# Kernel tuning notes

Hardware: AMD Instinct MI355X
Metric: run time of the kernel (lower is better)

The kernel has to match this reference:

```python
import jax, jax.numpy as jnp
import numpy as np

D_MODEL = 2048
NUM_HEADS = 16
HEAD_DIM = 128
ROPE_BASE = 10000.0
NEG_INF = -1e9


def setup_inputs() -> dict:
    key = jax.random.key(0)
    ks = jax.random.split(key, 5)
    B, S = 2, 2048
    hidden_states = jax.random.normal(ks[0], (B, S, D_MODEL), dtype=jnp.float32)
    # additive causal mask: 0 on/below diagonal, large-negative above
    causal = jnp.triu(jnp.full((S, S), NEG_INF, dtype=jnp.float32), k=1)
    attention_mask = jnp.broadcast_to(causal, (B, 1, S, S))
    position_ids = jnp.broadcast_to(jnp.arange(S, dtype=jnp.int32), (B, S))
    scale = 1.0 / np.sqrt(D_MODEL)
    Wq = jax.random.normal(ks[1], (D_MODEL, NUM_HEADS * HEAD_DIM), dtype=jnp.float32) * scale
    Wk = jax.random.normal(ks[2], (D_MODEL, NUM_HEADS * HEAD_DIM), dtype=jnp.float32) * scale
    Wv = jax.random.normal(ks[3], (D_MODEL, NUM_HEADS * HEAD_DIM), dtype=jnp.float32) * scale
    Wo = jax.random.normal(ks[4], (NUM_HEADS * HEAD_DIM, D_MODEL), dtype=jnp.float32) * scale
    return {"hidden_states": hidden_states, "attention_mask": attention_mask,
            "position_ids": position_ids, "Wq": Wq, "Wk": Wk, "Wv": Wv, "Wo": Wo}


def _rope_cos_sin(position_ids):
    # inv_freq: [head_dim/2]
    inv_freq = 1.0 / (ROPE_BASE ** (jnp.arange(0, HEAD_DIM, 2, dtype=jnp.float32) / HEAD_DIM))
    freqs = position_ids.astype(jnp.float32)[..., None] * inv_freq  # [B,S,hd/2]
    emb = jnp.concatenate([freqs, freqs], axis=-1)  # [B,S,hd]
    return jnp.cos(emb), jnp.sin(emb)


def _rotate_half(x):
    x1, x2 = jnp.split(x, 2, axis=-1)
    return jnp.concatenate([-x2, x1], axis=-1)


def reference(hidden_states, attention_mask, position_ids, Wq, Wk, Wv, Wo):
    B, S, _ = hidden_states.shape
    H, Dh = NUM_HEADS, HEAD_DIM
    q = (hidden_states @ Wq).reshape(B, S, H, Dh).transpose(0, 2, 1, 3)  # [B,H,S,Dh]
    k = (hidden_states @ Wk).reshape(B, S, H, Dh).transpose(0, 2, 1, 3)
    v = (hidden_states @ Wv).reshape(B, S, H, Dh).transpose(0, 2, 1, 3)
    cos, sin = _rope_cos_sin(position_ids)  # [B,S,Dh]
    cos = cos[:, None, :, :]  # [B,1,S,Dh]
    sin = sin[:, None, :, :]
    q = q * cos + _rotate_half(q) * sin
    k = k * cos + _rotate_half(k) * sin
    scaling = 1.0 / np.sqrt(Dh)
    scores = jnp.einsum('bhqd,bhkd->bhqk', q, k) * scaling  # [B,H,S,S]
    scores = scores + attention_mask[:, :, :, :S]
    attn = jax.nn.softmax(scores.astype(jnp.float32), axis=-1).astype(q.dtype)
    # dropout p=0.0 / eval mode -> identity
    out = jnp.einsum('bhqk,bhkd->bhqd', attn, v)  # [B,H,S,Dh]
    out = out.transpose(0, 2, 1, 3).reshape(B, S, H * Dh)
    return out @ Wo
```

## Files before the change

kernel.cpp:

```cpp
#include <hip/hip_runtime.h>

typedef __attribute__((ext_vector_type(4))) float f32x4;
typedef __attribute__((ext_vector_type(8))) _Float16 f16x8;
typedef __attribute__((ext_vector_type(4))) _Float16 f16x4;

#define SEQ 2048
#define DM 2048
#define NQKV 6144

__device__ __forceinline__ void gload16(const _Float16* g, _Float16* l) {
  __builtin_amdgcn_global_load_lds(
      (const __attribute__((address_space(1))) void*)g,
      (__attribute__((address_space(3))) void*)l, 16, 0, 0);
}

__global__ __launch_bounds__(256) void cvt_x_kernel(const float* __restrict__ X,
                                                    _Float16* __restrict__ Xb, int n4) {
  int i = blockIdx.x * 256 + threadIdx.x;
  if (i < n4) {
    const float4 v = ((const float4*)X)[i];
    f16x4 o;
    o.x = (_Float16)v.x; o.y = (_Float16)v.y; o.z = (_Float16)v.z; o.w = (_Float16)v.w;
    ((f16x4*)Xb)[i] = o;
  }
}

__global__ __launch_bounds__(256) void wtrans_all_kernel(const float* __restrict__ Wq,
                                                         const float* __restrict__ Wk,
                                                         const float* __restrict__ Wv,
                                                         const float* __restrict__ Wo,
                                                         _Float16* __restrict__ Wqkvt,
                                                         _Float16* __restrict__ Wot) {
  __shared__ float tile[64][65];
  const int z = blockIdx.z;
  const float* W = (z == 0) ? Wq : (z == 1) ? Wk : (z == 2) ? Wv : Wo;
  _Float16* Wt = (z < 3) ? (Wqkvt + (size_t)z * 2048 * 2048) : Wot;
  const int n0 = blockIdx.x * 64, k0 = blockIdx.y * 64;
  const int tx = threadIdx.x & 15, ty = threadIdx.x >> 4;
#pragma unroll
  for (int i = 0; i < 4; ++i) {
    const int r = ty + i * 16;
    const float4 v = *(const float4*)&W[(size_t)(k0 + r) * 2048 + n0 + tx * 4];
    tile[r][tx * 4] = v.x; tile[r][tx * 4 + 1] = v.y;
    tile[r][tx * 4 + 2] = v.z; tile[r][tx * 4 + 3] = v.w;
  }
  __syncthreads();
  const int r = threadIdx.x >> 2, u = threadIdx.x & 3;
  _Float16 o[16];
#pragma unroll
  for (int i = 0; i < 16; ++i) o[i] = (_Float16)tile[u * 16 + i][r];
  _Float16* dst = &Wt[(size_t)(n0 + r) * 2048 + k0 + u * 16];
  *(f16x8*)&dst[0] = *(f16x8*)&o[0];
  *(f16x8*)&dst[8] = *(f16x8*)&o[8];
}

__global__ __launch_bounds__(256) void rope_table_kernel(float* __restrict__ ct,
                                                         float* __restrict__ st) {
  int i = blockIdx.x * 256 + threadIdx.x;
  int pos = i >> 6, f = i & 63;
  float inv = powf(10000.0f, -(float)f / 64.0f);
  float ang = (float)pos * inv;
  ct[i] = cosf(ang);
  st[i] = sinf(ang);
}

template <int MODE>
__global__ __launch_bounds__(512, 2) void gemm8n_kernel(
    const _Float16* __restrict__ A, const _Float16* __restrict__ Bt,
    float* __restrict__ Cout, int M, int N, int K,
    const int* __restrict__ pos_ids, const float* __restrict__ ct,
    const float* __restrict__ st, _Float16* __restrict__ Qo,
    _Float16* __restrict__ Ko, _Float16* __restrict__ Vo) {
  __shared__ __align__(16) char smem[147456];
  _Float16* As = (_Float16*)smem;
  _Float16* Bs = (_Float16*)(smem + 98304);
  const int nwg = gridDim.x * gridDim.y;
  const int orig = blockIdx.y * gridDim.x + blockIdx.x;
  const int id = (orig & 7) * (nwg >> 3) + (orig >> 3);
  const int bx = id % gridDim.x, by = id / gridDim.x;
  const int bm = by * 256, bn = bx * 128;
  const int t = threadIdx.x, lane = t & 63, w = t >> 6;
  const int wm = w >> 2, wn = w & 3;
  const int rl = lane & 15, lr4 = lane >> 4;
  const int NKT = K >> 6;

  const int srow = t >> 3;
  const int scol = ((t & 7) ^ (srow & 7)) << 3;
  const _Float16* pA = A + (size_t)(bm + srow) * K + scol;
  const _Float16* pB = Bt + (size_t)(bn + srow) * K + scol;
  _Float16* lA = As + t * 8;
  _Float16* lB = Bs + t * 8;
  const size_t rowK64 = (size_t)64 * K;

#define STA(H, KT, SLOT)                                                   \
  { const size_t _g = (size_t)((H) * 128) * K + (size_t)(KT) * 64;         \
    gload16(pA + _g, lA + (SLOT) * 16384 + (H) * 8192);                    \
    gload16(pA + _g + rowK64, lA + (SLOT) * 16384 + (H) * 8192 + 4096); }
#define STB(KT, SLOT)                                                      \
  { const size_t _g = (size_t)(KT) * 64;                                   \
    gload16(pB + _g, lB + (SLOT) * 8192);                                  \
    gload16(pB + _g + rowK64, lB + (SLOT) * 8192 + 4096); }

  const int sw0 = (lr4 ^ (rl & 7)) << 3;
  const int sw1 = ((4 + lr4) ^ (rl & 7)) << 3;
  const int aoff = (wm * 64 + rl) * 64;
  const int boff = (wn * 32 + rl) * 64;

  f16x8 a_[4][2], b_[2][2];
  f32x4 acc[2][4][2];
#pragma unroll
  for (int qm = 0; qm < 2; ++qm)
#pragma unroll
    for (int mf = 0; mf < 4; ++mf)
#pragma unroll
      for (int nf = 0; nf < 2; ++nf) acc[qm][mf][nf] = (f32x4)0.0f;

#define LOAD_A(H, SLOT)                                                 \
  { const _Float16* _p = As + (SLOT) * 16384 + (H) * 8192 + aoff;       \
    _Pragma("unroll") for (int mf = 0; mf < 4; ++mf) {                  \
      a_[mf][0] = *(const f16x8*)&_p[mf * 1024 + sw0];                  \
      a_[mf][1] = *(const f16x8*)&_p[mf * 1024 + sw1]; } }
#define LOAD_B(SLOT)                                                    \
  { const _Float16* _p = Bs + (SLOT) * 8192 + boff;                     \
    _Pragma("unroll") for (int nf = 0; nf < 2; ++nf) {                  \
      b_[nf][0] = *(const f16x8*)&_p[nf * 1024 + sw0];                  \
      b_[nf][1] = *(const f16x8*)&_p[nf * 1024 + sw1]; } }
#define MFMA_Q(QM)                                                      \
  __builtin_amdgcn_s_setprio(1);                                        \
  _Pragma("unroll") for (int mf = 0; mf < 4; ++mf)                      \
    _Pragma("unroll") for (int nf = 0; nf < 2; ++nf) {                  \
      acc[QM][mf][nf] = __builtin_amdgcn_mfma_f32_16x16x32_f16(         \
          a_[mf][0], b_[nf][0], acc[QM][mf][nf], 0, 0, 0);              \
      acc[QM][mf][nf] = __builtin_amdgcn_mfma_f32_16x16x32_f16(         \
          a_[mf][1], b_[nf][1], acc[QM][mf][nf], 0, 0, 0); }            \
  __builtin_amdgcn_s_setprio(0);
#define BAR()                                                           \
  do { __builtin_amdgcn_sched_barrier(0); __builtin_amdgcn_s_barrier(); \
       __builtin_amdgcn_sched_barrier(0); } while (0)
#define LGKM0()                                                         \
  do { asm volatile("s_waitcnt lgkmcnt(0)" ::: "memory");               \
       __builtin_amdgcn_sched_barrier(0); } while (0)
#define VM6() asm volatile("s_waitcnt vmcnt(6)" ::: "memory")
#define VM0() asm volatile("s_waitcnt vmcnt(0)" ::: "memory")

  STA(0, 0, 0); STB(0, 0); STA(1, 0, 0);
  STA(0, 1, 1); STB(1, 1); STA(1, 1, 1);
  VM6();
  BAR();

  for (int jb = 0; jb + 4 < NKT; jb += 3) {
    LOAD_A(0, 0); LOAD_B(0); STA(0, jb + 2, 2); STB(jb + 2, 2);
    BAR(); LGKM0(); MFMA_Q(0); BAR();
    LOAD_A(1, 0); STA(1, jb + 2, 2);
    VM6(); BAR(); LGKM0(); MFMA_Q(1); BAR();
    LOAD_A(0, 1); LOAD_B(1); STA(0, jb + 3, 0); STB(jb + 3, 0);
    BAR(); LGKM0(); MFMA_Q(0); BAR();
    LOAD_A(1, 1); STA(1, jb + 3, 0);
    VM6(); BAR(); LGKM0(); MFMA_Q(1); BAR();
    LOAD_A(0, 2); LOAD_B(2); STA(0, jb + 4, 1); STB(jb + 4, 1);
    BAR(); LGKM0(); MFMA_Q(0); BAR();
    LOAD_A(1, 2); STA(1, jb + 4, 1);
    VM6(); BAR(); LGKM0(); MFMA_Q(1); BAR();
  }
  {
    LOAD_A(0, 0); LOAD_B(0);
    BAR(); LGKM0(); MFMA_Q(0); BAR();
    LOAD_A(1, 0);
    VM0();
    BAR(); LGKM0(); MFMA_Q(1); BAR();
    LOAD_A(0, 1); LOAD_B(1);
    BAR(); LGKM0(); MFMA_Q(0); BAR();
    LOAD_A(1, 1);
    BAR(); LGKM0(); MFMA_Q(1);
  }

  if (MODE == 0) {
#pragma unroll
    for (int qm = 0; qm < 2; ++qm)
#pragma unroll
      for (int mf = 0; mf < 4; ++mf)
#pragma unroll
        for (int nf = 0; nf < 2; ++nf) {
          const int col = bn + wn * 32 + nf * 16 + rl;
#pragma unroll
          for (int ri = 0; ri < 4; ++ri) {
            const int row = bm + qm * 128 + wm * 64 + mf * 16 + lr4 * 4 + ri;
            Cout[(size_t)row * N + col] = acc[qm][mf][nf][ri];
          }
        }
  } else {
    const int ttype = bx >> 4;
    const int hh = bx & 15;
    if (ttype == 2) {
#pragma unroll
      for (int qm = 0; qm < 2; ++qm)
#pragma unroll
        for (int mf = 0; mf < 4; ++mf)
#pragma unroll
          for (int nf = 0; nf < 2; ++nf) {
            const int d = wn * 32 + nf * 16 + rl;
            const int s0 = bm + qm * 128 + wm * 64 + mf * 16 + lr4 * 4;
            const int bb = s0 >> 11, ss = s0 & 2047;
            f16x4 v4;
#pragma unroll
            for (int ri = 0; ri < 4; ++ri) v4[ri] = (_Float16)acc[qm][mf][nf][ri];
            *(f16x4*)&Vo[((size_t)(bb * 16 + hh) * 128 + d) * SEQ + ss] = v4;
          }
    } else {
      float* cl = (float*)smem;
      LGKM0();
      BAR();
#pragma unroll
      for (int qm = 0; qm < 2; ++qm)
#pragma unroll
        for (int mf = 0; mf < 4; ++mf)
#pragma unroll
          for (int nf = 0; nf < 2; ++nf) {
            const int col = wn * 32 + nf * 16 + rl;
            const int r0 = qm * 128 + wm * 64 + mf * 16 + lr4 * 4;
#pragma unroll
            for (int ri = 0; ri < 4; ++ri) cl[(r0 + ri) * 130 + col] = acc[qm][mf][nf][ri];
          }
      BAR();
      const int row = t >> 1, pb = (t & 1) * 32;
      const int rg = bm + row;
      const int bb = rg >> 11, ss = rg & 2047;
      const int pos = pos_ids[rg];
      const float* cp = ct + pos * 64 + pb;
      const float* sp = st + pos * 64 + pb;
      _Float16* dst = (ttype ? Ko : Qo) + ((size_t)(bb * 16 + hh) * SEQ + ss) * 128;
      const float qs = ttype ? 1.0f : 0.08838834764831845f;
      const float* crow = cl + row * 130;
      _Float16 o1[32], o2[32];
#pragma unroll
      for (int i = 0; i < 32; ++i) {
        const float x1 = crow[pb + i], x2 = crow[pb + 64 + i];
        const float c = cp[i], s = sp[i];
        o1[i] = (_Float16)((x1 * c - x2 * s) * qs);
        o2[i] = (_Float16)((x2 * c + x1 * s) * qs);
      }
#pragma unroll
      for (int i = 0; i < 4; ++i) {
        *(f16x8*)&dst[pb + i * 8] = *(f16x8*)&o1[i * 8];
        *(f16x8*)&dst[pb + 64 + i * 8] = *(f16x8*)&o2[i * 8];
      }
    }
  }
#undef STA
#undef STB
#undef LOAD_A
#undef LOAD_B
#undef MFMA_Q
#undef BAR
#undef LGKM0
#undef VM6
#undef VM0
}

__global__ __launch_bounds__(512) void attn_kernel(const _Float16* __restrict__ Q,
                                                   const _Float16* __restrict__ K,
                                                   const _Float16* __restrict__ Vt,
                                                   _Float16* __restrict__ O) {
  __shared__ __align__(16) _Float16 Ks[2][128 * 128];
  __shared__ __align__(16) _Float16 Vs[2][128 * 128];
  __shared__ __align__(16) _Float16 Ps[8][16 * 128];
  const int bh = blockIdx.x;
  const int pair = blockIdx.y;
  const int b = bh >> 4, h = bh & 15;
  const int t = threadIdx.x, lane = t & 63, w = t >> 6;
  const int lr = lane >> 4, lc = lane & 15;
  const _Float16* Qb = Q + (size_t)bh * SEQ * 128;
  const _Float16* Kb = K + (size_t)bh * SEQ * 128;
  const _Float16* Vb = Vt + (size_t)bh * 128 * SEQ;

  f16x8 onef;
#pragma unroll
  for (int i = 0; i < 8; ++i) onef[i] = (_Float16)1.0f;

#define ABAR()                                                          \
  do { __builtin_amdgcn_sched_barrier(0); __builtin_amdgcn_s_barrier(); \
       __builtin_amdgcn_sched_barrier(0); } while (0)

  auto stage = [&](int buf, int kb) {
    const int k0 = kb * 128;
#pragma unroll
    for (int i = 0; i < 4; ++i) {
      const int c = i * 512 + t;
      const int row = c >> 4, u = c & 15;
      gload16(&Kb[(size_t)(k0 + row) * 128 + ((u ^ (row & 7)) << 3)], &Ks[buf][c * 8]);
    }
#pragma unroll
    for (int i = 0; i < 4; ++i) {
      const int c = i * 512 + t;
      const int dim = c >> 4, u = c & 15;
      gload16(&Vb[(size_t)dim * SEQ + k0 + ((u ^ (dim & 7)) << 3)], &Vs[buf][c * 8]);
    }
  };

  for (int half = 0; half < 2; ++half) {
    const int j = half ? (15 - pair) : pair;
    const int q0 = j * 128;
    const int nkb = j + 1;
    const int rowmin = q0 + w * 16;

    f16x8 qf[4];
    {
      const int qrow = q0 + w * 16 + lc;
#pragma unroll
      for (int kk = 0; kk < 4; ++kk)
        qf[kk] = *(const f16x8*)&Qb[(size_t)qrow * 128 + kk * 32 + lr * 8];
    }
    f32x4 acco[8];
#pragma unroll
    for (int i = 0; i < 8; ++i) acco[i] = (f32x4)0.0f;
    float l_r[4] = {0.f, 0.f, 0.f, 0.f};

    stage(0, 0);
    for (int kb = 0; kb < nkb; ++kb) {
      const int cur = kb & 1;
      const bool more = kb + 1 < nkb;
      if (more) {
        stage(cur ^ 1, kb + 1);
        asm volatile("s_waitcnt vmcnt(8)" ::: "memory");
      } else {
        asm volatile("s_waitcnt vmcnt(0)" ::: "memory");
      }
      ABAR();
      const int k0 = kb * 128;
      if (k0 <= rowmin + 15) {
        f32x4 sacc[8];
#pragma unroll
        for (int jj = 0; jj < 8; ++jj) sacc[jj] = (f32x4)0.0f;
#pragma unroll
        for (int jj = 0; jj < 8; ++jj) {
          const int krow = jj * 16 + lc;
#pragma unroll
          for (int kk = 0; kk < 4; ++kk) {
            const int idx = (krow * 128 + kk * 32 + lr * 8) ^ ((krow & 7) << 3);
            f16x8 kf = *(const f16x8*)&Ks[cur][idx];
            sacc[jj] = __builtin_amdgcn_mfma_f32_16x16x32_f16(qf[kk], kf, sacc[jj], 0, 0, 0);
          }
        }
        const bool diag = (k0 + 127 > rowmin);
#pragma unroll
        for (int r = 0; r < 4; ++r) {
          const int rowi = rowmin + lr * 4 + r;
          const int rbase = (lr * 4 + r) * 128;
          const int rsw = ((lr * 4 + r) & 7) << 3;
#pragma unroll
          for (int jj = 0; jj < 8; ++jj) {
            float sv = sacc[jj][r];
            if (diag && (k0 + jj * 16 + lc > rowi)) sv = -1e30f;
            const float pv = __expf(sv);
            Ps[w][rbase + ((jj * 16 + lc) ^ rsw)] = (_Float16)pv;
          }
        }
        const int csw = (lc & 7) << 3;
        f16x8 pf[4];
#pragma unroll
        for (int c = 0; c < 4; ++c)
          pf[c] = *(const f16x8*)&Ps[w][lc * 128 + ((c * 32 + lr * 8) ^ csw)];
        f32x4 psum = (f32x4)0.0f;
#pragma unroll
        for (int c = 0; c < 4; ++c)
          psum = __builtin_amdgcn_mfma_f32_16x16x32_f16(pf[c], onef, psum, 0, 0, 0);
#pragma unroll
        for (int tt = 0; tt < 8; ++tt) {
          const int dim = tt * 16 + lc;
          const int dsw = (dim & 7) << 3;
#pragma unroll
          for (int c = 0; c < 4; ++c) {
            const int vidx = (dim * 128 + c * 32 + lr * 8) ^ dsw;
            acco[tt] = __builtin_amdgcn_mfma_f32_16x16x32_f16(
                pf[c], *(const f16x8*)&Vs[cur][vidx], acco[tt], 0, 0, 0);
          }
        }
#pragma unroll
        for (int r = 0; r < 4; ++r) l_r[r] += psum[r];
      }
      ABAR();
    }
#pragma unroll
    for (int tt = 0; tt < 8; ++tt) {
      const int col = h * 128 + tt * 16 + lc;
#pragma unroll
      for (int r = 0; r < 4; ++r) {
        const int row = q0 + w * 16 + lr * 4 + r;
        O[(size_t)(b * SEQ + row) * DM + col] = (_Float16)(acco[tt][r] / l_r[r]);
      }
    }
  }
#undef ABAR
}

extern "C" void kernel_launch(void* const* d_in, const int* in_sizes, int n_in,
                              void* d_out, int out_size, void* d_ws, size_t ws_size,
                              hipStream_t stream) {
  const float* hidden = (const float*)d_in[0];
  const int* pos_ids = (const int*)d_in[2];
  const float* Wq = (const float*)d_in[3];
  const float* Wk = (const float*)d_in[4];
  const float* Wv = (const float*)d_in[5];
  const float* Wo = (const float*)d_in[6];

  char* ws = (char*)d_ws;
  _Float16* Xb    = (_Float16*)(ws + 0);
  _Float16* Wqkvt = (_Float16*)(ws + 16777216);
  _Float16* Wot   = (_Float16*)(ws + 41943040);
  _Float16* Qbuf  = (_Float16*)(ws + 50331648);
  _Float16* Kbuf  = (_Float16*)(ws + 67108864);
  _Float16* Vtbuf = (_Float16*)(ws + 83886080);
  _Float16* Obuf  = (_Float16*)(ws + 100663296);
  float* ct       = (float*)(ws + 117440512);
  float* st       = (float*)(ws + 117964800);

  cvt_x_kernel<<<8192, 256, 0, stream>>>(hidden, Xb, 2097152);
  wtrans_all_kernel<<<dim3(32, 32, 4), 256, 0, stream>>>(Wq, Wk, Wv, Wo, Wqkvt, Wot);
  rope_table_kernel<<<512, 256, 0, stream>>>(ct, st);

  gemm8n_kernel<1><<<dim3(48, 16), 512, 0, stream>>>(
      Xb, Wqkvt, nullptr, 4096, 6144, 2048, pos_ids, ct, st, Qbuf, Kbuf, Vtbuf);

  attn_kernel<<<dim3(32, 8), 512, 0, stream>>>(Qbuf, Kbuf, Vtbuf, Obuf);

  gemm8n_kernel<0><<<dim3(16, 16), 512, 0, stream>>>(
      Obuf, Wot, (float*)d_out, 4096, 2048, 2048, nullptr, nullptr, nullptr,
      nullptr, nullptr, nullptr);
}
```

Baseline: 257.5 us.

## Use 256x256 tiles with double-buffered schedule for fused QKV projection GEMM

Adds a dedicated QKV GEMM kernel that computes 256x256 output tiles per workgroup, covering two heads, instead of 256x128. It uses a two-stage LDS buffer with interleaved A/B loads and keeps two sets of B fragments in registers. The aim is to cut global and LDS traffic per FLOP and to halve the grid to 384 workgroups. The RoPE/V-transpose epilogue is reworked to handle two heads per tile in two passes. The cost is more accumulator registers (128 floats per thread), which risks spills or lower occupancy, and less pipeline depth.

```diff
diff --git a/kernel.cpp b/kernel.cpp
--- a/kernel.cpp
+++ b/kernel.cpp
@@ -64,16 +64,217 @@
   st[i] = sinf(ang);
 }
 
-template <int MODE>
+#define BARX()                                                          \
+  do { __builtin_amdgcn_sched_barrier(0); __builtin_amdgcn_s_barrier(); \
+       __builtin_amdgcn_sched_barrier(0); } while (0)
+#define LGKM0X()                                                        \
+  do { asm volatile("s_waitcnt lgkmcnt(0)" ::: "memory");               \
+       __builtin_amdgcn_sched_barrier(0); } while (0)
+
+__global__ __launch_bounds__(512, 2) void gemm8q_kernel(
+    const _Float16* __restrict__ A, const _Float16* __restrict__ Bt,
+    int M, int N, int K, const int* __restrict__ pos_ids,
+    const float* __restrict__ ct, const float* __restrict__ st,
+    _Float16* __restrict__ Qo, _Float16* __restrict__ Ko,
+    _Float16* __restrict__ Vo) {
+  __shared__ __align__(16) char smem[135168];
+  _Float16* As = (_Float16*)smem;
+  _Float16* Bs = (_Float16*)(smem + 65536);
+  const int nwg = gridDim.x * gridDim.y;
+  const int orig = blockIdx.y * gridDim.x + blockIdx.x;
+  const int id = (orig & 7) * (nwg >> 3) + (orig >> 3);
+  const int bx = id % gridDim.x, by = id / gridDim.x;
+  const int bm = by * 256, bn = bx * 256;
+  const int t = threadIdx.x, lane = t & 63, w = t >> 6;
+  const int wm = w >> 2, wn = w & 3;
+  const int rl = lane & 15, lr4 = lane >> 4;
+  const int NKT = K >> 6;
+
+  const int srow = t >> 3;
+  const int scol = ((t & 7) ^ (srow & 7)) << 3;
+  const _Float16* pA = A + (size_t)(bm + srow) * K + scol;
+  const _Float16* pB = Bt + (size_t)(bn + srow) * K + scol;
+  _Float16* lA = As + t * 8;
+  _Float16* lB = Bs + t * 8;
+  const size_t rowK64 = (size_t)64 * K;
+
+#define STA(H, KT, BUF)                                                    \
+  { const size_t _g = (size_t)((H) * 128) * K + (size_t)(KT) * 64;         \
+    gload16(pA + _g, lA + (BUF) * 16384 + (H) * 8192);                     \
+    gload16(pA + _g + rowK64, lA + (BUF) * 16384 + (H) * 8192 + 4096); }
+#define STB(H, KT, BUF)                                                    \
+  { const size_t _g = (size_t)((H) * 128) * K + (size_t)(KT) * 64;         \
+    gload16(pB + _g, lB + (BUF) * 16384 + (H) * 8192);                     \
+    gload16(pB + _g + rowK64, lB + (BUF) * 16384 + (H) * 8192 + 4096); }
+
+  const int sw0 = (lr4 ^ (rl & 7)) << 3;
+  const int sw1 = ((4 + lr4) ^ (rl & 7)) << 3;
+  const int aoff = (wm * 64 + rl) * 64;
+  const int boff = (wn * 32 + rl) * 64;
+
+  f16x8 a_[4][2], b0_[2][2], b1_[2][2];
+  f32x4 acc[2][2][4][2];
+#pragma unroll
+  for (int qm = 0; qm < 2; ++qm)
+#pragma unroll
+    for (int qn = 0; qn < 2; ++qn)
+#pragma unroll
+      for (int mf = 0; mf < 4; ++mf)
+#pragma unroll
+        for (int nf = 0; nf < 2; ++nf) acc[qm][qn][mf][nf] = (f32x4)0.0f;
+
+#define LOAD_A(QM, BUF)                                                 \
+  { const _Float16* _p = As + (BUF) * 16384 + (QM) * 8192 + aoff;       \
+    _Pragma("unroll") for (int mf = 0; mf < 4; ++mf) {                  \
+      a_[mf][0] = *(const f16x8*)&_p[mf * 1024 + sw0];                  \
+      a_[mf][1] = *(const f16x8*)&_p[mf * 1024 + sw1]; } }
+#define LOAD_B(DST, QN, BUF)                                            \
+  { const _Float16* _p = Bs + (BUF) * 16384 + (QN) * 8192 + boff;       \
+    _Pragma("unroll") for (int nf = 0; nf < 2; ++nf) {                  \
+      DST[nf][0] = *(const f16x8*)&_p[nf * 1024 + sw0];                 \
+      DST[nf][1] = *(const f16x8*)&_p[nf * 1024 + sw1]; } }
+#define MFMA_Q(QM, QN, BREG)                                            \
+  __builtin_amdgcn_s_setprio(1);                                        \
+  _Pragma("unroll") for (int mf = 0; mf < 4; ++mf)                      \
+    _Pragma("unroll") for (int nf = 0; nf < 2; ++nf) {                  \
+      acc[QM][QN][mf][nf] = __builtin_amdgcn_mfma_f32_16x16x32_f16(     \
+          a_[mf][0], BREG[nf][0], acc[QM][QN][mf][nf], 0, 0, 0);        \
+      acc[QM][QN][mf][nf] = __builtin_amdgcn_mfma_f32_16x16x32_f16(     \
+          a_[mf][1], BREG[nf][1], acc[QM][QN][mf][nf], 0, 0, 0); }      \
+  __builtin_amdgcn_s_setprio(0);
+
+  STA(0, 0, 0); STB(0, 0, 0); STA(1, 0, 0); STB(1, 0, 0);
+  STA(0, 1, 1); STB(0, 1, 1); STA(1, 1, 1);
+  asm volatile("s_waitcnt vmcnt(6)" ::: "memory");
+  BARX();
+  LOAD_B(b0_, 0, 0);
+
+  for (int i = 0; i < (NKT >> 1) - 1; ++i) {
+    const int k1 = 2 * i + 1, k2 = 2 * i + 2, k3 = 2 * i + 3;
+    LOAD_A(0, 0); STB(1, k1, 1);
+    BARX(); LGKM0X(); MFMA_Q(0, 0, b0_); BARX();
+    LOAD_B(b1_, 1, 0); STA(0, k2, 0);
+    BARX(); LGKM0X(); MFMA_Q(0, 1, b1_); BARX();
+    LOAD_A(1, 0); STB(0, k2, 0);
+    BARX(); LGKM0X(); MFMA_Q(1, 0, b0_); BARX();
+    STA(1, k2, 0);
+    asm volatile("s_waitcnt vmcnt(6)" ::: "memory");
+    BARX();
+    MFMA_Q(1, 1, b1_);
+    LOAD_B(b0_, 0, 1);
+    BARX();
+    LOAD_A(0, 1); STB(1, k2, 0);
+    BARX(); LGKM0X(); MFMA_Q(0, 0, b0_); BARX();
+    LOAD_B(b1_, 1, 1); STA(0, k3, 1);
+    BARX(); LGKM0X(); MFMA_Q(0, 1, b1_); BARX();
+    LOAD_A(1, 1); STB(0, k3, 1);
+    BARX(); LGKM0X(); MFMA_Q(1, 0, b0_); BARX();
+    STA(1, k3, 1);
+    asm volatile("s_waitcnt vmcnt(6)" ::: "memory");
+    BARX();
+    MFMA_Q(1, 1, b1_);
+    LOAD_B(b0_, 0, 0);
+    BARX();
+  }
+  {
+    const int k1 = NKT - 1;
+    LOAD_A(0, 0); STB(1, k1, 1);
+    BARX(); LGKM0X(); MFMA_Q(0, 0, b0_); BARX();
+    LOAD_B(b1_, 1, 0);
+    BARX(); LGKM0X(); MFMA_Q(0, 1, b1_); BARX();
+    LOAD_A(1, 0);
+    BARX(); LGKM0X(); MFMA_Q(1, 0, b0_); BARX();
+    asm volatile("s_waitcnt vmcnt(0)" ::: "memory");
+    BARX();
+    MFMA_Q(1, 1, b1_);
+    LOAD_B(b0_, 0, 1);
+    BARX();
+    LOAD_A(0, 1);
+    BARX(); LGKM0X(); MFMA_Q(0, 0, b0_); BARX();
+    LOAD_B(b1_, 1, 1);
+    BARX(); LGKM0X(); MFMA_Q(0, 1, b1_); BARX();
+    LOAD_A(1, 1);
+    BARX(); LGKM0X(); MFMA_Q(1, 0, b0_); BARX();
+    MFMA_Q(1, 1, b1_);
+  }
+
+  const int ttype = bx >> 3;
+  const int hh2 = (bx & 7) * 2;
+  if (ttype == 2) {
+#pragma unroll
+    for (int qm = 0; qm < 2; ++qm)
+#pragma unroll
+      for (int qn = 0; qn < 2; ++qn)
+#pragma unroll
+        for (int mf = 0; mf < 4; ++mf)
+#pragma unroll
+          for (int nf = 0; nf < 2; ++nf) {
+            const int head = hh2 + qn;
+            const int d = wn * 32 + nf * 16 + rl;
+            const int s0 = bm + qm * 128 + wm * 64 + mf * 16 + lr4 * 4;
+            const int bb = s0 >> 11, ss = s0 & 2047;
+            f16x4 v4;
+#pragma unroll
+            for (int ri = 0; ri < 4; ++ri) v4[ri] = (_Float16)acc[qm][qn][mf][nf][ri];
+            *(f16x4*)&Vo[((size_t)(bb * 16 + head) * 128 + d) * SEQ + ss] = v4;
+          }
+  } else {
+    float* cl = (float*)smem;
+    LGKM0X();
+    BARX();
+#pragma unroll
+    for (int qm = 0; qm < 2; ++qm) {
+#pragma unroll
+      for (int qn = 0; qn < 2; ++qn)
+#pragma unroll
+        for (int mf = 0; mf < 4; ++mf)
+#pragma unroll
+          for (int nf = 0; nf < 2; ++nf) {
+            const int col = qn * 128 + wn * 32 + nf * 16 + rl;
+            const int r0 = wm * 64 + mf * 16 + lr4 * 4;
+#pragma unroll
+            for (int ri = 0; ri < 4; ++ri)
+              cl[(r0 + ri) * 264 + col] = acc[qm][qn][mf][nf][ri];
+          }
+      BARX();
+      const int row_l = t >> 2, head_i = (t >> 1) & 1, pb = (t & 1) * 32;
+      const int rg = bm + qm * 128 + row_l;
+      const int bb = rg >> 11, ss = rg & 2047;
+      const int pos = pos_ids[rg];
+      const float* cp = ct + pos * 64 + pb;
+      const float* sp = st + pos * 64 + pb;
+      const int head = hh2 + head_i;
+      _Float16* dst = (ttype ? Ko : Qo) + ((size_t)(bb * 16 + head) * SEQ + ss) * 128;
+      const float qs = ttype ? 1.0f : 0.08838834764831845f;
+      const float* crow = cl + row_l * 264 + head_i * 128;
+      _Float16 o1[32], o2[32];
+#pragma unroll
+      for (int i = 0; i < 32; ++i) {
+        const float x1 = crow[pb + i], x2 = crow[pb + 64 + i];
+        const float c = cp[i], s = sp[i];
+        o1[i] = (_Float16)((x1 * c - x2 * s) * qs);
+        o2[i] = (_Float16)((x2 * c + x1 * s) * qs);
+      }
+#pragma unroll
+      for (int i = 0; i < 4; ++i) {
+        *(f16x8*)&dst[pb + i * 8] = *(f16x8*)&o1[i * 8];
+        *(f16x8*)&dst[pb + 64 + i * 8] = *(f16x8*)&o2[i * 8];
+      }
+      BARX();
+    }
+  }
+#undef STA
+#undef STB
+#undef LOAD_A
+#undef LOAD_B
+#undef MFMA_Q
+}
+
 __global__ __launch_bounds__(512, 2) void gemm8n_kernel(
     const _Float16* __restrict__ A, const _Float16* __restrict__ Bt,
-    float* __restrict__ Cout, int M, int N, int K,
-    const int* __restrict__ pos_ids, const float* __restrict__ ct,
-    const float* __restrict__ st, _Float16* __restrict__ Qo,
-    _Float16* __restrict__ Ko, _Float16* __restrict__ Vo) {
-  __shared__ __align__(16) char smem[147456];
-  _Float16* As = (_Float16*)smem;
-  _Float16* Bs = (_Float16*)(smem + 98304);
+    float* __restrict__ Cout, int M, int N, int K) {
+  __shared__ __align__(16) _Float16 As[3 * 16384];
+  __shared__ __align__(16) _Float16 Bs[3 * 8192];
   const int nwg = gridDim.x * gridDim.y;
   const int orig = blockIdx.y * gridDim.x + blockIdx.x;
   const int id = (orig & 7) * (nwg >> 3) + (orig >> 3);
@@ -134,125 +335,58 @@
       acc[QM][mf][nf] = __builtin_amdgcn_mfma_f32_16x16x32_f16(         \
           a_[mf][1], b_[nf][1], acc[QM][mf][nf], 0, 0, 0); }            \
   __builtin_amdgcn_s_setprio(0);
-#define BAR()                                                           \
-  do { __builtin_amdgcn_sched_barrier(0); __builtin_amdgcn_s_barrier(); \
-       __builtin_amdgcn_sched_barrier(0); } while (0)
-#define LGKM0()                                                         \
-  do { asm volatile("s_waitcnt lgkmcnt(0)" ::: "memory");               \
-       __builtin_amdgcn_sched_barrier(0); } while (0)
 #define VM6() asm volatile("s_waitcnt vmcnt(6)" ::: "memory")
 #define VM0() asm volatile("s_waitcnt vmcnt(0)" ::: "memory")
 
   STA(0, 0, 0); STB(0, 0); STA(1, 0, 0);
   STA(0, 1, 1); STB(1, 1); STA(1, 1, 1);
   VM6();
-  BAR();
+  BARX();
 
   for (int jb = 0; jb + 4 < NKT; jb += 3) {
     LOAD_A(0, 0); LOAD_B(0); STA(0, jb + 2, 2); STB(jb + 2, 2);
-    BAR(); LGKM0(); MFMA_Q(0); BAR();
+    BARX(); LGKM0X(); MFMA_Q(0); BARX();
     LOAD_A(1, 0); STA(1, jb + 2, 2);
-    VM6(); BAR(); LGKM0(); MFMA_Q(1); BAR();
+    VM6(); BARX(); LGKM0X(); MFMA_Q(1); BARX();
     LOAD_A(0, 1); LOAD_B(1); STA(0, jb + 3, 0); STB(jb + 3, 0);
-    BAR(); LGKM0(); MFMA_Q(0); BAR();
+    BARX(); LGKM0X(); MFMA_Q(0); BARX();
     LOAD_A(1, 1); STA(1, jb + 3, 0);
-    VM6(); BAR(); LGKM0(); MFMA_Q(1); BAR();
+    VM6(); BARX(); LGKM0X(); MFMA_Q(1); BARX();
     LOAD_A(0, 2); LOAD_B(2); STA(0, jb + 4, 1); STB(jb + 4, 1);
-    BAR(); LGKM0(); MFMA_Q(0); BAR();
+    BARX(); LGKM0X(); MFMA_Q(0); BARX();
     LOAD_A(1, 2); STA(1, jb + 4, 1);
-    VM6(); BAR(); LGKM0(); MFMA_Q(1); BAR();
+    VM6(); BARX(); LGKM0X(); MFMA_Q(1); BARX();
   }
   {
     LOAD_A(0, 0); LOAD_B(0);
-    BAR(); LGKM0(); MFMA_Q(0); BAR();
+    BARX(); LGKM0X(); MFMA_Q(0); BARX();
     LOAD_A(1, 0);
     VM0();
-    BAR(); LGKM0(); MFMA_Q(1); BAR();
+    BARX(); LGKM0X(); MFMA_Q(1); BARX();
     LOAD_A(0, 1); LOAD_B(1);
-    BAR(); LGKM0(); MFMA_Q(0); BAR();
+    BARX(); LGKM0X(); MFMA_Q(0); BARX();
     LOAD_A(1, 1);
-    BAR(); LGKM0(); MFMA_Q(1);
-  }
-
-  if (MODE == 0) {
-#pragma unroll
-    for (int qm = 0; qm < 2; ++qm)
-#pragma unroll
-      for (int mf = 0; mf < 4; ++mf)
-#pragma unroll
-        for (int nf = 0; nf < 2; ++nf) {
-          const int col = bn + wn * 32 + nf * 16 + rl;
-#pragma unroll
-          for (int ri = 0; ri < 4; ++ri) {
-            const int row = bm + qm * 128 + wm * 64 + mf * 16 + lr4 * 4 + ri;
-            Cout[(size_t)row * N + col] = acc[qm][mf][nf][ri];
-          }
+    BARX(); LGKM0X(); MFMA_Q(1);
+  }
+
+#pragma unroll
+  for (int qm = 0; qm < 2; ++qm)
+#pragma unroll
+    for (int mf = 0; mf < 4; ++mf)
+#pragma unroll
+      for (int nf = 0; nf < 2; ++nf) {
+        const int col = bn + wn * 32 + nf * 16 + rl;
+#pragma unroll
+        for (int ri = 0; ri < 4; ++ri) {
+          const int row = bm + qm * 128 + wm * 64 + mf * 16 + lr4 * 4 + ri;
+          Cout[(size_t)row * N + col] = acc[qm][mf][nf][ri];
         }
-  } else {
-    const int ttype = bx >> 4;
-    const int hh = bx & 15;
-    if (ttype == 2) {
-#pragma unroll
-      for (int qm = 0; qm < 2; ++qm)
-#pragma unroll
-        for (int mf = 0; mf < 4; ++mf)
-#pragma unroll
-          for (int nf = 0; nf < 2; ++nf) {
-            const int d = wn * 32 + nf * 16 + rl;
-            const int s0 = bm + qm * 128 + wm * 64 + mf * 16 + lr4 * 4;
-            const int bb = s0 >> 11, ss = s0 & 2047;
-            f16x4 v4;
-#pragma unroll
-            for (int ri = 0; ri < 4; ++ri) v4[ri] = (_Float16)acc[qm][mf][nf][ri];
-            *(f16x4*)&Vo[((size_t)(bb * 16 + hh) * 128 + d) * SEQ + ss] = v4;
-          }
-    } else {
-      float* cl = (float*)smem;
-      LGKM0();
-      BAR();
-#pragma unroll
-      for (int qm = 0; qm < 2; ++qm)
-#pragma unroll
-        for (int mf = 0; mf < 4; ++mf)
-#pragma unroll
-          for (int nf = 0; nf < 2; ++nf) {
-            const int col = wn * 32 + nf * 16 + rl;
-            const int r0 = qm * 128 + wm * 64 + mf * 16 + lr4 * 4;
-#pragma unroll
-            for (int ri = 0; ri < 4; ++ri) cl[(r0 + ri) * 130 + col] = acc[qm][mf][nf][ri];
-          }
-      BAR();
-      const int row = t >> 1, pb = (t & 1) * 32;
-      const int rg = bm + row;
-      const int bb = rg >> 11, ss = rg & 2047;
-      const int pos = pos_ids[rg];
-      const float* cp = ct + pos * 64 + pb;
-      const float* sp = st + pos * 64 + pb;
-      _Float16* dst = (ttype ? Ko : Qo) + ((size_t)(bb * 16 + hh) * SEQ + ss) * 128;
-      const float qs = ttype ? 1.0f : 0.08838834764831845f;
-      const float* crow = cl + row * 130;
-      _Float16 o1[32], o2[32];
-#pragma unroll
-      for (int i = 0; i < 32; ++i) {
-        const float x1 = crow[pb + i], x2 = crow[pb + 64 + i];
-        const float c = cp[i], s = sp[i];
-        o1[i] = (_Float16)((x1 * c - x2 * s) * qs);
-        o2[i] = (_Float16)((x2 * c + x1 * s) * qs);
       }
-#pragma unroll
-      for (int i = 0; i < 4; ++i) {
-        *(f16x8*)&dst[pb + i * 8] = *(f16x8*)&o1[i * 8];
-        *(f16x8*)&dst[pb + 64 + i * 8] = *(f16x8*)&o2[i * 8];
-      }
-    }
-  }
 #undef STA
 #undef STB
 #undef LOAD_A
 #undef LOAD_B
 #undef MFMA_Q
-#undef BAR
-#undef LGKM0
 #undef VM6
 #undef VM0
 }
@@ -277,10 +411,6 @@
 #pragma unroll
   for (int i = 0; i < 8; ++i) onef[i] = (_Float16)1.0f;
 
-#define ABAR()                                                          \
-  do { __builtin_amdgcn_sched_barrier(0); __builtin_amdgcn_s_barrier(); \
-       __builtin_amdgcn_sched_barrier(0); } while (0)
-
   auto stage = [&](int buf, int kb) {
     const int k0 = kb * 128;
 #pragma unroll
@@ -325,7 +455,7 @@
       } else {
         asm volatile("s_waitcnt vmcnt(0)" ::: "memory");
       }
-      ABAR();
+      BARX();
       const int k0 = kb * 128;
       if (k0 <= rowmin + 15) {
         f32x4 sacc[8];
@@ -378,7 +508,7 @@
 #pragma unroll
         for (int r = 0; r < 4; ++r) l_r[r] += psum[r];
       }
-      ABAR();
+      BARX();
     }
 #pragma unroll
     for (int tt = 0; tt < 8; ++tt) {
@@ -390,7 +520,6 @@
       }
     }
   }
-#undef ABAR
 }
 
 extern "C" void kernel_launch(void* const* d_in, const int* in_sizes, int n_in,
@@ -418,12 +547,11 @@
   wtrans_all_kernel<<<dim3(32, 32, 4), 256, 0, stream>>>(Wq, Wk, Wv, Wo, Wqkvt, Wot);
   rope_table_kernel<<<512, 256, 0, stream>>>(ct, st);
 
-  gemm8n_kernel<1><<<dim3(48, 16), 512, 0, stream>>>(
-      Xb, Wqkvt, nullptr, 4096, 6144, 2048, pos_ids, ct, st, Qbuf, Kbuf, Vtbuf);
+  gemm8q_kernel<<<dim3(24, 16), 512, 0, stream>>>(
+      Xb, Wqkvt, 4096, 6144, 2048, pos_ids, ct, st, Qbuf, Kbuf, Vtbuf);
 
   attn_kernel<<<dim3(32, 8), 512, 0, stream>>>(Qbuf, Kbuf, Vtbuf, Obuf);
 
-  gemm8n_kernel<0><<<dim3(16, 16), 512, 0, stream>>>(
-      Obuf, Wot, (float*)d_out, 4096, 2048, 2048, nullptr, nullptr, nullptr,
-      nullptr, nullptr, nullptr);
-}
+  gemm8n_kernel<<<dim3(16, 16), 512, 0, stream>>>(
+      Obuf, Wot, (float*)d_out, 4096, 2048, 2048);
+}
```

After: 256.1 us. About the same (-0.6%).

## Restructure attention kernel to 32x32 MFMA with split key/dim halves per wave

Applied to the files above, without the earlier changes.

The attention kernel moves from 16x16x32 MFMAs, where each wave owned 16 query rows, to 32x32x16 MFMAs. Each wave now covers 32 query rows and half of the keys or output dims, and the 128x128 probability tile is shared through LDS. The S=K·Q^T product is computed transposed so each wave writes its half of P, followed by a barrier before P·V. The aim is to cut LDS traffic per MFMA and improve matrix-core efficiency, at the cost of an extra block-wide barrier per key tile and the loss of per-wave skipping of fully masked key tiles. The GEMM barrier macros are only renamed so they can be shared.

```diff
diff --git a/kernel.cpp b/kernel.cpp
--- a/kernel.cpp
+++ b/kernel.cpp
@@ -1,6 +1,7 @@
 #include <hip/hip_runtime.h>
 
 typedef __attribute__((ext_vector_type(4))) float f32x4;
+typedef __attribute__((ext_vector_type(16))) float f32x16;
 typedef __attribute__((ext_vector_type(8))) _Float16 f16x8;
 typedef __attribute__((ext_vector_type(4))) _Float16 f16x4;
 
@@ -63,6 +64,13 @@
   ct[i] = cosf(ang);
   st[i] = sinf(ang);
 }
+
+#define BARX()                                                          \
+  do { __builtin_amdgcn_sched_barrier(0); __builtin_amdgcn_s_barrier(); \
+       __builtin_amdgcn_sched_barrier(0); } while (0)
+#define LGKM0X()                                                        \
+  do { asm volatile("s_waitcnt lgkmcnt(0)" ::: "memory");               \
+       __builtin_amdgcn_sched_barrier(0); } while (0)
 
 template <int MODE>
 __global__ __launch_bounds__(512, 2) void gemm8n_kernel(
@@ -134,44 +142,38 @@
       acc[QM][mf][nf] = __builtin_amdgcn_mfma_f32_16x16x32_f16(         \
           a_[mf][1], b_[nf][1], acc[QM][mf][nf], 0, 0, 0); }            \
   __builtin_amdgcn_s_setprio(0);
-#define BAR()                                                           \
-  do { __builtin_amdgcn_sched_barrier(0); __builtin_amdgcn_s_barrier(); \
-       __builtin_amdgcn_sched_barrier(0); } while (0)
-#define LGKM0()                                                         \
-  do { asm volatile("s_waitcnt lgkmcnt(0)" ::: "memory");               \
-       __builtin_amdgcn_sched_barrier(0); } while (0)
 #define VM6() asm volatile("s_waitcnt vmcnt(6)" ::: "memory")
 #define VM0() asm volatile("s_waitcnt vmcnt(0)" ::: "memory")
 
   STA(0, 0, 0); STB(0, 0); STA(1, 0, 0);
   STA(0, 1, 1); STB(1, 1); STA(1, 1, 1);
   VM6();
-  BAR();
+  BARX();
 
   for (int jb = 0; jb + 4 < NKT; jb += 3) {
     LOAD_A(0, 0); LOAD_B(0); STA(0, jb + 2, 2); STB(jb + 2, 2);
-    BAR(); LGKM0(); MFMA_Q(0); BAR();
+    BARX(); LGKM0X(); MFMA_Q(0); BARX();
     LOAD_A(1, 0); STA(1, jb + 2, 2);
-    VM6(); BAR(); LGKM0(); MFMA_Q(1); BAR();
+    VM6(); BARX(); LGKM0X(); MFMA_Q(1); BARX();
     LOAD_A(0, 1); LOAD_B(1); STA(0, jb + 3, 0); STB(jb + 3, 0);
-    BAR(); LGKM0(); MFMA_Q(0); BAR();
+    BARX(); LGKM0X(); MFMA_Q(0); BARX();
     LOAD_A(1, 1); STA(1, jb + 3, 0);
-    VM6(); BAR(); LGKM0(); MFMA_Q(1); BAR();
+    VM6(); BARX(); LGKM0X(); MFMA_Q(1); BARX();
     LOAD_A(0, 2); LOAD_B(2); STA(0, jb + 4, 1); STB(jb + 4, 1);
-    BAR(); LGKM0(); MFMA_Q(0); BAR();
+    BARX(); LGKM0X(); MFMA_Q(0); BARX();
     LOAD_A(1, 2); STA(1, jb + 4, 1);
-    VM6(); BAR(); LGKM0(); MFMA_Q(1); BAR();
+    VM6(); BARX(); LGKM0X(); MFMA_Q(1); BARX();
   }
   {
     LOAD_A(0, 0); LOAD_B(0);
-    BAR(); LGKM0(); MFMA_Q(0); BAR();
+    BARX(); LGKM0X(); MFMA_Q(0); BARX();
     LOAD_A(1, 0);
     VM0();
-    BAR(); LGKM0(); MFMA_Q(1); BAR();
+    BARX(); LGKM0X(); MFMA_Q(1); BARX();
     LOAD_A(0, 1); LOAD_B(1);
-    BAR(); LGKM0(); MFMA_Q(0); BAR();
+    BARX(); LGKM0X(); MFMA_Q(0); BARX();
     LOAD_A(1, 1);
-    BAR(); LGKM0(); MFMA_Q(1);
+    BARX(); LGKM0X(); MFMA_Q(1);
   }
 
   if (MODE == 0) {
@@ -208,8 +210,8 @@
           }
     } else {
       float* cl = (float*)smem;
-      LGKM0();
-      BAR();
+      LGKM0X();
+      BARX();
 #pragma unroll
       for (int qm = 0; qm < 2; ++qm)
 #pragma unroll
@@ -221,7 +223,7 @@
 #pragma unroll
             for (int ri = 0; ri < 4; ++ri) cl[(r0 + ri) * 130 + col] = acc[qm][mf][nf][ri];
           }
-      BAR();
+      BARX();
       const int row = t >> 1, pb = (t & 1) * 32;
       const int rg = bm + row;
       const int bb = rg >> 11, ss = rg & 2047;
@@ -251,8 +253,6 @@
 #undef LOAD_A
 #undef LOAD_B
 #undef MFMA_Q
-#undef BAR
-#undef LGKM0
 #undef VM6
 #undef VM0
 }
@@ -263,12 +263,13 @@
                                                    _Float16* __restrict__ O) {
   __shared__ __align__(16) _Float16 Ks[2][128 * 128];
   __shared__ __align__(16) _Float16 Vs[2][128 * 128];
-  __shared__ __align__(16) _Float16 Ps[8][16 * 128];
+  __shared__ __align__(16) _Float16 Ps[128 * 128];
   const int bh = blockIdx.x;
   const int pair = blockIdx.y;
   const int b = bh >> 4, h = bh & 15;
   const int t = threadIdx.x, lane = t & 63, w = t >> 6;
-  const int lr = lane >> 4, lc = lane & 15;
+  const int rowgrp = w & 3, kh = w >> 2;
+  const int l31 = lane & 31, l5 = lane >> 5;
   const _Float16* Qb = Q + (size_t)bh * SEQ * 128;
   const _Float16* Kb = K + (size_t)bh * SEQ * 128;
   const _Float16* Vb = Vt + (size_t)bh * 128 * SEQ;
@@ -276,10 +277,6 @@
   f16x8 onef;
 #pragma unroll
   for (int i = 0; i < 8; ++i) onef[i] = (_Float16)1.0f;
-
-#define ABAR()                                                          \
-  do { __builtin_amdgcn_sched_barrier(0); __builtin_amdgcn_s_barrier(); \
-       __builtin_amdgcn_sched_barrier(0); } while (0)
 
   auto stage = [&](int buf, int kb) {
     const int k0 = kb * 128;
@@ -301,96 +298,90 @@
     const int j = half ? (15 - pair) : pair;
     const int q0 = j * 128;
     const int nkb = j + 1;
-    const int rowmin = q0 + w * 16;
-
-    f16x8 qf[4];
-    {
-      const int qrow = q0 + w * 16 + lc;
-#pragma unroll
-      for (int kk = 0; kk < 4; ++kk)
-        qf[kk] = *(const f16x8*)&Qb[(size_t)qrow * 128 + kk * 32 + lr * 8];
-    }
-    f32x4 acco[8];
-#pragma unroll
-    for (int i = 0; i < 8; ++i) acco[i] = (f32x4)0.0f;
-    float l_r[4] = {0.f, 0.f, 0.f, 0.f};
+
+    const int prow = rowgrp * 32 + l31;
+    const int qrow = q0 + prow;
+    f16x8 qf[8];
+#pragma unroll
+    for (int kc = 0; kc < 8; ++kc)
+      qf[kc] = *(const f16x8*)&Qb[(size_t)qrow * 128 + kc * 16 + l5 * 8];
+
+    f32x16 acco0 = (f32x16)0.0f, acco1 = (f32x16)0.0f, lsum = (f32x16)0.0f;
 
     stage(0, 0);
     for (int kb = 0; kb < nkb; ++kb) {
       const int cur = kb & 1;
-      const bool more = kb + 1 < nkb;
-      if (more) {
+      if (kb + 1 < nkb) {
         stage(cur ^ 1, kb + 1);
         asm volatile("s_waitcnt vmcnt(8)" ::: "memory");
       } else {
         asm volatile("s_waitcnt vmcnt(0)" ::: "memory");
       }
-      ABAR();
+      BARX();
       const int k0 = kb * 128;
-      if (k0 <= rowmin + 15) {
-        f32x4 sacc[8];
-#pragma unroll
-        for (int jj = 0; jj < 8; ++jj) sacc[jj] = (f32x4)0.0f;
-#pragma unroll
-        for (int jj = 0; jj < 8; ++jj) {
-          const int krow = jj * 16 + lc;
-#pragma unroll
-          for (int kk = 0; kk < 4; ++kk) {
-            const int idx = (krow * 128 + kk * 32 + lr * 8) ^ ((krow & 7) << 3);
-            f16x8 kf = *(const f16x8*)&Ks[cur][idx];
-            sacc[jj] = __builtin_amdgcn_mfma_f32_16x16x32_f16(qf[kk], kf, sacc[jj], 0, 0, 0);
+      f32x16 sacc0 = (f32x16)0.0f, sacc1 = (f32x16)0.0f;
+      const int key0 = kh * 64 + l31;
+      const int ksw = (l31 & 7) << 3;
+#pragma unroll
+      for (int kc = 0; kc < 8; ++kc) {
+        const int off = kc * 16 + l5 * 8;
+        sacc0 = __builtin_amdgcn_mfma_f32_32x32x16_f16(
+            *(const f16x8*)&Ks[cur][key0 * 128 + (off ^ ksw)], qf[kc], sacc0, 0, 0, 0);
+        sacc1 = __builtin_amdgcn_mfma_f32_32x32x16_f16(
+            *(const f16x8*)&Ks[cur][(key0 + 32) * 128 + (off ^ ksw)], qf[kc], sacc1, 0, 0, 0);
+      }
+      const bool diag = (kb == j);
+      const int rsw = (prow & 7) << 3;
+#pragma unroll
+      for (int kb2 = 0; kb2 < 2; ++kb2) {
+        const int kbase = kh * 64 + kb2 * 32;
+#pragma unroll
+        for (int g = 0; g < 4; ++g) {
+          f16x4 p4;
+#pragma unroll
+          for (int e = 0; e < 4; ++e) {
+            const int reg = g * 4 + e;
+            float sv = kb2 ? sacc1[reg] : sacc0[reg];
+            if (diag) {
+              const int key_l = kbase + g * 8 + 4 * l5 + e;
+              if (k0 + key_l > q0 + prow) sv = -1e30f;
+            }
+            p4[e] = (_Float16)__expf(sv);
           }
+          const int key4 = kbase + g * 8 + 4 * l5;
+          *(f16x4*)&Ps[prow * 128 + (key4 ^ rsw)] = p4;
         }
-        const bool diag = (k0 + 127 > rowmin);
-#pragma unroll
-        for (int r = 0; r < 4; ++r) {
-          const int rowi = rowmin + lr * 4 + r;
-          const int rbase = (lr * 4 + r) * 128;
-          const int rsw = ((lr * 4 + r) & 7) << 3;
-#pragma unroll
-          for (int jj = 0; jj < 8; ++jj) {
-            float sv = sacc[jj][r];
-            if (diag && (k0 + jj * 16 + lc > rowi)) sv = -1e30f;
-            const float pv = __expf(sv);
-            Ps[w][rbase + ((jj * 16 + lc) ^ rsw)] = (_Float16)pv;
-          }
-        }
-        const int csw = (lc & 7) << 3;
-        f16x8 pf[4];
-#pragma unroll
-        for (int c = 0; c < 4; ++c)
-          pf[c] = *(const f16x8*)&Ps[w][lc * 128 + ((c * 32 + lr * 8) ^ csw)];
-        f32x4 psum = (f32x4)0.0f;
-#pragma unroll
-        for (int c = 0; c < 4; ++c)
-          psum = __builtin_amdgcn_mfma_f32_16x16x32_f16(pf[c], onef, psum, 0, 0, 0);
-#pragma unroll
-        for (int tt = 0; tt < 8; ++tt) {
-          const int dim = tt * 16 + lc;
-          const int dsw = (dim & 7) << 3;
-#pragma unroll
-          for (int c = 0; c < 4; ++c) {
-            const int vidx = (dim * 128 + c * 32 + lr * 8) ^ dsw;
-            acco[tt] = __builtin_amdgcn_mfma_f32_16x16x32_f16(
-                pf[c], *(const f16x8*)&Vs[cur][vidx], acco[tt], 0, 0, 0);
-          }
-        }
-#pragma unroll
-        for (int r = 0; r < 4; ++r) l_r[r] += psum[r];
-      }
-      ABAR();
+      }
+      LGKM0X();
+      BARX();
+      f16x8 pA[8];
+#pragma unroll
+      for (int kc = 0; kc < 8; ++kc)
+        pA[kc] = *(const f16x8*)&Ps[prow * 128 + ((kc * 16 + l5 * 8) ^ rsw)];
+#pragma unroll
+      for (int kc = 0; kc < 8; ++kc)
+        lsum = __builtin_amdgcn_mfma_f32_32x32x16_f16(pA[kc], onef, lsum, 0, 0, 0);
+      const int d0 = kh * 64 + l31;
+      const int dsw = (l31 & 7) << 3;
+#pragma unroll
+      for (int kc = 0; kc < 8; ++kc) {
+        const int off = kc * 16 + l5 * 8;
+        acco0 = __builtin_amdgcn_mfma_f32_32x32x16_f16(
+            pA[kc], *(const f16x8*)&Vs[cur][d0 * 128 + (off ^ dsw)], acco0, 0, 0, 0);
+        acco1 = __builtin_amdgcn_mfma_f32_32x32x16_f16(
+            pA[kc], *(const f16x8*)&Vs[cur][(d0 + 32) * 128 + (off ^ dsw)], acco1, 0, 0, 0);
+      }
+      BARX();
     }
 #pragma unroll
-    for (int tt = 0; tt < 8; ++tt) {
-      const int col = h * 128 + tt * 16 + lc;
-#pragma unroll
-      for (int r = 0; r < 4; ++r) {
-        const int row = q0 + w * 16 + lr * 4 + r;
-        O[(size_t)(b * SEQ + row) * DM + col] = (_Float16)(acco[tt][r] / l_r[r]);
-      }
+    for (int reg = 0; reg < 16; ++reg) {
+      const int row = q0 + rowgrp * 32 + (reg & 3) + 8 * (reg >> 2) + 4 * l5;
+      const float inv = 1.0f / lsum[reg];
+      _Float16* orow = &O[(size_t)(b * SEQ + row) * DM + h * 128 + kh * 64 + l31];
+      orow[0] = (_Float16)(acco0[reg] * inv);
+      orow[32] = (_Float16)(acco1[reg] * inv);
     }
   }
-#undef ABAR
 }
 
 extern "C" void kernel_launch(void* const* d_in, const int* in_sizes, int n_in,
```

Measured after the change: 245.6 us, median of 2. 4.6% less time.
